# Kernel tuning notes

Measured on AMD Instinct MI355X. Metric: run time of the kernel, lower is better.

The kernel has to match this reference:

```python
import jax, jax.numpy as jnp
import numpy as np

N, C, L = 4, 256, 4096
RED, NH, CHUNK = 4, 4, 64
HB = min(L // CHUNK + (L // CHUNK) % 2, 128)  # 64 hash buckets
EPS_BN = 1e-5
EPS_NORM = 5e-5
RES_SCALE = 1.0


def _bn(x, g, b, m, v):
    # inference batchnorm over channel dim of [N, C, L]
    scale = g / jnp.sqrt(v + EPS_BN)
    return (x - m[None, :, None]) * scale[None, :, None] + b[None, :, None]


def _conv1d(x, w, pad):
    return jax.lax.conv_general_dilated(x, w, (1,), [(pad, pad)],
                                        dimension_numbers=('NCH', 'OIH', 'NCH'))


def setup_inputs() -> dict:
    key = jax.random.key(0)
    ks = jax.random.split(key, 4)
    Cr = C // RED
    return {
        'x': jax.random.normal(ks[0], (N, C, L), jnp.float32),
        'rot': jax.random.normal(ks[1], (Cr, NH, HB // 2), jnp.float32),
        'w_match': jax.random.normal(ks[2], (Cr, C, 3), jnp.float32) * 0.05,
        'bn1_g': jnp.ones((Cr,), jnp.float32), 'bn1_b': jnp.zeros((Cr,), jnp.float32),
        'bn1_m': jnp.zeros((Cr,), jnp.float32), 'bn1_v': jnp.ones((Cr,), jnp.float32),
        'w_asm': jax.random.normal(ks[3], (C, C, 1), jnp.float32) * 0.05,
        'bn2_g': jnp.ones((C,), jnp.float32), 'bn2_b': jnp.zeros((C,), jnp.float32),
        'bn2_m': jnp.zeros((C,), jnp.float32), 'bn2_v': jnp.ones((C,), jnp.float32),
        'bn3_g': jnp.ones((C,), jnp.float32), 'bn3_b': jnp.zeros((C,), jnp.float32),
        'bn3_m': jnp.zeros((C,), jnp.float32), 'bn3_v': jnp.ones((C,), jnp.float32),
    }


def reference(x, rot, w_match, bn1_g, bn1_b, bn1_m, bn1_v,
              w_asm, bn2_g, bn2_b, bn2_m, bn2_v,
              bn3_g, bn3_b, bn3_m, bn3_v):
    Cr = C // RED
    # conv_match / conv_assembly branches (conv -> BN -> ReLU)
    x_embed = jax.nn.relu(_bn(_conv1d(x, w_match, 1), bn1_g, bn1_b, bn1_m, bn1_v))  # [N,Cr,L]
    y_embed = jax.nn.relu(_bn(_conv1d(x, w_asm, 0), bn2_g, bn2_b, bn2_m, bn2_v))    # [N,C,L]
    x_embed = jnp.transpose(x_embed, (0, 2, 1))  # [N,L,Cr]
    y_embed = jnp.transpose(y_embed, (0, 2, 1))  # [N,L,C]

    # --- LSH hashing: random rotations, cat with negation, argmax bucket ---
    rv = jnp.einsum('ntf,fhi->nhti', x_embed, rot)           # [N,NH,L,HB/2]
    rv = jnp.concatenate([rv, -rv], axis=-1)                  # [N,NH,L,HB]
    codes = jnp.argmax(rv, axis=-1)                           # [N,NH,L]
    codes = codes + jnp.arange(NH, dtype=codes.dtype)[None, :, None]
    codes = codes.reshape(N, NH * L)

    indices = jnp.argsort(codes, axis=-1)
    undo_sort = jnp.argsort(indices, axis=-1)
    mod_idx = indices % L

    xs = jnp.take_along_axis(x_embed, mod_idx[:, :, None], axis=1)  # [N,NH*L,Cr]
    ys = jnp.take_along_axis(y_embed, mod_idx[:, :, None], axis=1)  # [N,NH*L,C]

    nchunks = L // CHUNK  # L divisible by CHUNK -> padding == 0
    xb = xs.reshape(N, NH, nchunks, CHUNK, Cr)
    yb = ys.reshape(N, NH, nchunks, CHUNK, C)

    # F.normalize(p=2, eps=5e-5): x / max(||x||, eps)
    nrm = jnp.linalg.norm(xb, axis=-1, keepdims=True)
    xm = xb / jnp.maximum(nrm, EPS_NORM)

    def adj(t):  # concat current, previous, next bucket along in-chunk axis
        return jnp.concatenate([t, jnp.roll(t, 1, axis=2), jnp.roll(t, -1, axis=2)], axis=3)

    xm = adj(xm)      # [N,NH,K,3*CHUNK,Cr]
    yb3 = adj(yb)     # [N,NH,K,3*CHUNK,C]

    raw = jnp.einsum('bhkie,bhkje->bhkij', xb, xm)            # [N,NH,K,CHUNK,3*CHUNK]
    lse = jax.scipy.special.logsumexp(raw, axis=-1, keepdims=True)
    score = jnp.exp(raw - lse)
    att = jnp.einsum('bhkij,bhkje->bhkie', score, yb3)        # [N,NH,K,CHUNK,C]

    att = att.reshape(N, NH * L, C)
    att = jnp.take_along_axis(att, undo_sort[:, :, None], axis=1).reshape(N, NH, L, C)
    # NOTE: original code does NOT undo-sort bucket_score; replicate faithfully
    bscore = lse.reshape(N, NH, L, 1)
    probs = jax.nn.softmax(bscore, axis=1)
    out = jnp.sum(att * probs, axis=1)                        # [N,L,C]
    out = jnp.transpose(out, (0, 2, 1))                       # [N,C,L]
    out = _bn(out, bn3_g, bn3_b, bn3_m, bn3_v) * RES_SCALE + x
    return out
```

## Files before the change

kernel.cpp:

```cpp
#include <hip/hip_runtime.h>
#include <math.h>

#define NN 4
#define CCH 256
#define LLEN 4096
#define NHEAD 4
#define NHL 16384
#define NBINS 67

typedef __attribute__((ext_vector_type(8))) short bshort8;
typedef __attribute__((ext_vector_type(4))) float f32x4;

__device__ __forceinline__ float4 f4fma(float4 a, float4 b, float4 c) {
  c.x = fmaf(a.x, b.x, c.x);
  c.y = fmaf(a.y, b.y, c.y);
  c.z = fmaf(a.z, b.z, c.z);
  c.w = fmaf(a.w, b.w, c.w);
  return c;
}
__device__ __forceinline__ float4 f4fmas(float s, float4 b, float4 c) {
  c.x = fmaf(s, b.x, c.x);
  c.y = fmaf(s, b.y, c.y);
  c.z = fmaf(s, b.z, c.z);
  c.w = fmaf(s, b.w, c.w);
  return c;
}
__device__ __forceinline__ unsigned short f2bf(float f) {
  union { float f; unsigned u; } v; v.f = f;
  unsigned r = v.u + 0x7FFF + ((v.u >> 16) & 1);
  return (unsigned short)(r >> 16);
}

__global__ __launch_bounds__(256, 2) void k_conv_match(
    const float* __restrict__ x, const float* __restrict__ w,
    const float* __restrict__ g, const float* __restrict__ b,
    const float* __restrict__ m, const float* __restrict__ v,
    float* __restrict__ xe) {
  __shared__ float xs[64 * 68];
  __shared__ float wl[64 * 193];
  const int tid = threadIdx.x;
  const int n = blockIdx.x >> 6;
  const int l0 = (blockIdx.x & 63) << 6;
  const float* xn = x + (size_t)n * CCH * LLEN;
  const int co = tid & 63;
  const int dlg = tid >> 6;
  float acc[16];
#pragma unroll
  for (int q = 0; q < 16; ++q) acc[q] = 0.f;
  for (int cc = 0; cc < 4; ++cc) {
    __syncthreads();
    for (int idx = tid; idx < 64 * 66; idx += 256) {
      int ci = idx / 66, j = idx - ci * 66;
      int l = l0 + j - 1;
      xs[ci * 68 + j] = (l >= 0 && l < LLEN) ? xn[(cc * 64 + ci) * LLEN + l] : 0.f;
    }
    for (int idx = tid; idx < 12288; idx += 256) {
      int cw = idx / 192, r = idx - cw * 192;
      wl[cw * 193 + r] = w[cw * 768 + cc * 192 + r];
    }
    __syncthreads();
    const float* wbase = &wl[co * 193];
    for (int cil = 0; cil < 64; ++cil) {
      const float* xrow = &xs[cil * 68 + dlg * 16];
      float4 p0 = ((const float4*)xrow)[0];
      float4 p1 = ((const float4*)xrow)[1];
      float4 p2 = ((const float4*)xrow)[2];
      float4 p3 = ((const float4*)xrow)[3];
      float4 p4 = ((const float4*)xrow)[4];
      float xr[20] = {p0.x,p0.y,p0.z,p0.w, p1.x,p1.y,p1.z,p1.w,
                      p2.x,p2.y,p2.z,p2.w, p3.x,p3.y,p3.z,p3.w,
                      p4.x,p4.y,p4.z,p4.w};
      float w0 = wbase[cil*3], w1 = wbase[cil*3+1], w2 = wbase[cil*3+2];
#pragma unroll
      for (int q = 0; q < 16; ++q) {
        acc[q] = fmaf(w0, xr[q], acc[q]);
        acc[q] = fmaf(w1, xr[q+1], acc[q]);
        acc[q] = fmaf(w2, xr[q+2], acc[q]);
      }
    }
  }
  float scale = g[co] * rsqrtf(v[co] + 1e-5f);
  float bias = b[co] - m[co] * scale;
  float* xo = xe + ((size_t)n * LLEN + l0) * 64 + co;
#pragma unroll
  for (int q = 0; q < 16; ++q) {
    float val = acc[q] * scale + bias;
    xo[(dlg * 16 + q) * 64] = val > 0.f ? val : 0.f;
  }
}

__global__ __launch_bounds__(256, 3) void k_conv_asm(
    const float* __restrict__ x, const float* __restrict__ w,
    const float* __restrict__ g, const float* __restrict__ b,
    const float* __restrict__ m, const float* __restrict__ v,
    float* __restrict__ ye) {
  __shared__ float xt[64 * 68];
  __shared__ float wt[64 * 132];
  const int tid = threadIdx.x;
  const int n = blockIdx.x >> 6;
  const int l0 = (blockIdx.x & 63) << 6;
  const int cg = tid & 31, lt = tid >> 5;
  float4 a0[8], a1[8];
#pragma unroll
  for (int q = 0; q < 8; ++q) { a0[q] = make_float4(0,0,0,0); a1[q] = make_float4(0,0,0,0); }
  for (int cc = 0; cc < 4; ++cc) {
    __syncthreads();
    for (int idx = tid; idx < 4096; idx += 256) {
      int ci = idx >> 6, dl = idx & 63;
      xt[ci * 68 + dl] = x[((size_t)n * 256 + cc * 64 + ci) * 4096 + l0 + dl];
    }
    for (int idx = tid; idx < 8192; idx += 256) {
      int ci = idx & 63, cl = idx >> 6;
      int c = ((cl >> 2) << 3) + (cl & 3);
      wt[ci * 132 + cl] = w[c * 256 + cc * 64 + ci];
    }
    __syncthreads();
    for (int ci = 0; ci < 64; ++ci) {
      const float4 xv0 = *(const float4*)&xt[ci * 68 + lt * 8];
      const float4 xv1 = *(const float4*)&xt[ci * 68 + lt * 8 + 4];
      const float4 w0 = *(const float4*)&wt[ci * 132 + cg * 4];
      float xl[8] = {xv0.x, xv0.y, xv0.z, xv0.w, xv1.x, xv1.y, xv1.z, xv1.w};
#pragma unroll
      for (int q = 0; q < 8; ++q) a0[q] = f4fmas(xl[q], w0, a0[q]);
    }
    __syncthreads();
    for (int idx = tid; idx < 8192; idx += 256) {
      int ci = idx & 63, cl = idx >> 6;
      int c = ((cl >> 2) << 3) + 4 + (cl & 3);
      wt[ci * 132 + cl] = w[c * 256 + cc * 64 + ci];
    }
    __syncthreads();
    for (int ci = 0; ci < 64; ++ci) {
      const float4 xv0 = *(const float4*)&xt[ci * 68 + lt * 8];
      const float4 xv1 = *(const float4*)&xt[ci * 68 + lt * 8 + 4];
      const float4 w1 = *(const float4*)&wt[ci * 132 + cg * 4];
      float xl[8] = {xv0.x, xv0.y, xv0.z, xv0.w, xv1.x, xv1.y, xv1.z, xv1.w};
#pragma unroll
      for (int q = 0; q < 8; ++q) a1[q] = f4fmas(xl[q], w1, a1[q]);
    }
  }
  const int c0 = cg * 8;
  float sc[8], bs[8];
#pragma unroll
  for (int u = 0; u < 8; ++u) {
    float s = g[c0+u] * rsqrtf(v[c0+u] + 1e-5f);
    sc[u] = s; bs[u] = b[c0+u] - m[c0+u] * s;
  }
#pragma unroll
  for (int q = 0; q < 8; ++q) {
    int l = l0 + lt * 8 + q;
    float4 o0, o1;
    o0.x = fmaxf(a0[q].x*sc[0]+bs[0], 0.f);
    o0.y = fmaxf(a0[q].y*sc[1]+bs[1], 0.f);
    o0.z = fmaxf(a0[q].z*sc[2]+bs[2], 0.f);
    o0.w = fmaxf(a0[q].w*sc[3]+bs[3], 0.f);
    o1.x = fmaxf(a1[q].x*sc[4]+bs[4], 0.f);
    o1.y = fmaxf(a1[q].y*sc[5]+bs[5], 0.f);
    o1.z = fmaxf(a1[q].z*sc[6]+bs[6], 0.f);
    o1.w = fmaxf(a1[q].w*sc[7]+bs[7], 0.f);
    float4* dst = (float4*)(ye + ((size_t)n * LLEN + l) * 256 + c0);
    dst[0] = o0; dst[1] = o1;
  }
}

__global__ __launch_bounds__(256) void k_codes(
    const float* __restrict__ xe, const float* __restrict__ rot,
    int* __restrict__ codes) {
  __shared__ float xsh[64 * 65];
  const int tid = threadIdx.x;
  const int n = blockIdx.x >> 6;
  const int t0 = (blockIdx.x & 63) << 6;
  for (int idx = tid; idx < 4096; idx += 256) {
    int tt = idx >> 6, f = idx & 63;
    xsh[tt * 65 + f] = xe[((size_t)n * LLEN + t0 + tt) * 64 + f];
  }
  __syncthreads();
  const int tt = tid & 63, h = tid >> 6;
  float rvv[32];
#pragma unroll
  for (int i = 0; i < 32; ++i) rvv[i] = 0.f;
  const float* xr = &xsh[tt * 65];
  for (int f = 0; f < 64; ++f) {
    float xf = xr[f];
    const float* rr = rot + ((f << 2) + h) * 32;
#pragma unroll
    for (int i = 0; i < 32; ++i) rvv[i] = fmaf(xf, rr[i], rvv[i]);
  }
  float best = rvv[0]; int bi = 0;
#pragma unroll
  for (int i = 1; i < 32; ++i) { if (rvv[i] > best) { best = rvv[i]; bi = i; } }
#pragma unroll
  for (int i = 0; i < 32; ++i) { float nv = -rvv[i]; if (nv > best) { best = nv; bi = 32 + i; } }
  codes[n * NHL + h * LLEN + t0 + tt] = bi + h;
}

__global__ __launch_bounds__(256) void k_hist(const int* __restrict__ codes,
                                              int* __restrict__ offs) {
  __shared__ int hist[NBINS];
  const int tid = threadIdx.x;
  const int n = blockIdx.x;
  if (tid < NBINS) hist[tid] = 0;
  __syncthreads();
  const int* cp = codes + n * NHL;
  for (int idx = tid; idx < NHL; idx += 256) atomicAdd(&hist[cp[idx]], 1);
  __syncthreads();
  if (tid == 0) {
    int s = 0;
    for (int c = 0; c < NBINS; ++c) { offs[n * (NBINS + 1) + c] = s; s += hist[c]; }
    offs[n * (NBINS + 1) + NBINS] = s;
  }
}

__global__ __launch_bounds__(64) void k_scatter(const int* __restrict__ codes,
                                                const int* __restrict__ offs,
                                                int* __restrict__ sidx,
                                                int* __restrict__ undo) {
  const int n = blockIdx.x / NBINS;
  const int c = blockIdx.x - n * NBINS;
  const int lane = threadIdx.x;
  const int* cp = codes + n * NHL;
  int base = offs[n * (NBINS + 1) + c];
  for (int ch = 0; ch < NHL / 64; ++ch) {
    int j = (ch << 6) + lane;
    int cv = cp[j];
    unsigned long long mk = __ballot(cv == c);
    if (cv == c) {
      int pos = base + __popcll(mk & ((1ull << lane) - 1ull));
      sidx[n * NHL + pos] = j;
      undo[n * NHL + j] = pos;
    }
    base += __popcll(mk);
  }
}

__global__ __launch_bounds__(256, 2) void k_att2(const float* __restrict__ xe,
                                                 const float* __restrict__ ye,
                                                 const int* __restrict__ sidx,
                                                 float* __restrict__ lseg,
                                                 float* __restrict__ att) {
  __shared__ float score[64 * 193];
  __shared__ float stg[4608];
  __shared__ int   tmap[192];
  __shared__ float rinv_c[64];
  __shared__ float psum[256];
  __shared__ float pm[256], ps[256];
  __shared__ float lse_row[64];
  const int tid = threadIdx.x;
  const int blk = blockIdx.x;
  const int n = blk >> 8, h = (blk >> 6) & 3, k = blk & 63;
  if (tid < 192) {
    int jl = tid & 63;
    int chn = (tid < 64) ? k : ((tid < 128) ? ((k + 63) & 63) : ((k + 1) & 63));
    tmap[tid] = sidx[n * NHL + h * LLEN + chn * 64 + jl] & (LLEN - 1);
  }
  __syncthreads();
  const float* xen = xe + (size_t)n * LLEN * 64;
  const int il = tid & 63, jg = tid >> 6;
  float4 xi[16];
  float ml = -1e30f, sl = 0.f;
  for (int jc = 0; jc < 3; ++jc) {
    if (jc) __syncthreads();
    {
      int r = tid >> 2, c0 = (tid & 3) * 16;
      const float4* src = (const float4*)(xen + (size_t)tmap[jc * 64 + r] * 64 + c0);
      float4* dst = (float4*)&stg[r * 68 + c0];
      dst[0] = src[0]; dst[1] = src[1]; dst[2] = src[2]; dst[3] = src[3];
    }
    __syncthreads();
    {
      int prt = tid >> 6;
      const float4* row = (const float4*)&stg[il * 68 + prt * 16];
      float s = 0.f;
#pragma unroll
      for (int u = 0; u < 4; ++u) {
        float4 vv = row[u];
        s += vv.x*vv.x + vv.y*vv.y + vv.z*vv.z + vv.w*vv.w;
      }
      psum[il * 4 + prt] = s;
    }
    __syncthreads();
    if (tid < 64) {
      float s = psum[tid*4] + psum[tid*4+1] + psum[tid*4+2] + psum[tid*4+3];
      rinv_c[tid] = 1.f / fmaxf(sqrtf(s), 5e-5f);
    }
    if (jc == 0) {
      const float4* xr = (const float4*)&stg[il * 68];
#pragma unroll
      for (int u = 0; u < 16; ++u) xi[u] = xr[u];
    }
    __syncthreads();
    for (int jj = 0; jj < 16; ++jj) {
      int jl2 = jg * 16 + jj;
      const float4* xj = (const float4*)&stg[jl2 * 68];
      float4 d4 = make_float4(0, 0, 0, 0);
#pragma unroll
      for (int u = 0; u < 16; ++u) d4 = f4fma(xi[u], xj[u], d4);
      float d = (d4.x + d4.y + d4.z + d4.w) * rinv_c[jl2];
      score[il * 193 + jc * 64 + jl2] = d;
      if (d > ml) { sl = sl * __expf(ml - d) + 1.f; ml = d; }
      else sl += __expf(d - ml);
    }
  }
  pm[il * 4 + jg] = ml; ps[il * 4 + jg] = sl;
  __syncthreads();
  if (tid < 64) {
    float m0 = pm[tid*4], m1 = pm[tid*4+1], m2 = pm[tid*4+2], m3 = pm[tid*4+3];
    float mm = fmaxf(fmaxf(m0, m1), fmaxf(m2, m3));
    float ss = ps[tid*4]  * __expf(m0 - mm) + ps[tid*4+1] * __expf(m1 - mm)
             + ps[tid*4+2] * __expf(m2 - mm) + ps[tid*4+3] * __expf(m3 - mm);
    float lv = mm + __logf(ss);
    lse_row[tid] = lv;
    lseg[n * NHL + h * LLEN + k * 64 + tid] = lv;
  }
  __syncthreads();
  float pbuf[48];
  {
    float lv = lse_row[il];
#pragma unroll
    for (int jc2 = 0; jc2 < 3; ++jc2)
#pragma unroll
      for (int jj = 0; jj < 16; ++jj)
        pbuf[jc2 * 16 + jj] = __expf(score[il * 193 + jc2 * 64 + jg * 16 + jj] - lv);
  }
  __syncthreads();
  {
    unsigned short* sb = (unsigned short*)score;
#pragma unroll
    for (int jc2 = 0; jc2 < 3; ++jc2)
#pragma unroll
      for (int jj = 0; jj < 16; ++jj) {
        int j = jc2 * 64 + jg * 16 + jj;
        sb[il * 200 + j] = f2bf(pbuf[jc2 * 16 + jj]);
      }
  }
  const int wv = tid >> 6, l = tid & 63;
  f32x4 acc[16];
#pragma unroll
  for (int ct = 0; ct < 16; ++ct) acc[ct] = (f32x4){0.f, 0.f, 0.f, 0.f};
  const unsigned short* sb = (const unsigned short*)score;
  unsigned short* ysh = (unsigned short*)stg;
  const float* yen = ye + (size_t)n * LLEN * 256;
  for (int kk = 0; kk < 6; ++kk) {
    __syncthreads();
    {
      int jl = tid & 31, c0 = (tid >> 5) * 32;
      const float4* src = (const float4*)(yen + (size_t)tmap[kk * 32 + jl] * 256 + c0);
#pragma unroll
      for (int u = 0; u < 8; ++u) {
        float4 yv = src[u];
        ysh[(c0 + u*4 + 0) * 32 + jl] = f2bf(yv.x);
        ysh[(c0 + u*4 + 1) * 32 + jl] = f2bf(yv.y);
        ysh[(c0 + u*4 + 2) * 32 + jl] = f2bf(yv.z);
        ysh[(c0 + u*4 + 3) * 32 + jl] = f2bf(yv.w);
      }
    }
    __syncthreads();
    bshort8 af = *(const bshort8*)&sb[(wv * 16 + (l & 15)) * 200 + kk * 32 + (l >> 4) * 8];
#pragma unroll
    for (int ct = 0; ct < 16; ++ct) {
      bshort8 bf = *(const bshort8*)&ysh[(ct * 16 + (l & 15)) * 32 + (l >> 4) * 8];
      acc[ct] = __builtin_amdgcn_mfma_f32_16x16x32_bf16(af, bf, acc[ct], 0, 0, 0);
    }
  }
  float* abase = att + ((size_t)n * NHL + h * LLEN + k * 64) * 256;
#pragma unroll
  for (int ct = 0; ct < 16; ++ct) {
    int c = ct * 16 + (l & 15);
    int i0 = wv * 16 + (l >> 4) * 4;
#pragma unroll
    for (int r = 0; r < 4; ++r)
      abase[(size_t)(i0 + r) * 256 + c] = acc[ct][r];
  }
}

__global__ __launch_bounds__(256, 2) void k_final3(const float* __restrict__ att,
                                                   const int* __restrict__ undo,
                                                   const float* __restrict__ lse,
                                                   const float* __restrict__ x,
                                                   const float* __restrict__ g,
                                                   const float* __restrict__ b,
                                                   const float* __restrict__ m,
                                                   const float* __restrict__ v,
                                                   float* __restrict__ out) {
  __shared__ float t[32 * 257];
  __shared__ float wts[32 * 4];
  __shared__ int   pos[32 * 4];
  const int tid = threadIdx.x;
  const int n = blockIdx.x >> 7;
  const int l0 = (blockIdx.x & 127) << 5;
  if (tid < 32) {
    int l = l0 + tid;
    float e0 = lse[n * NHL + l];
    float e1 = lse[n * NHL + LLEN + l];
    float e2 = lse[n * NHL + 2 * LLEN + l];
    float e3 = lse[n * NHL + 3 * LLEN + l];
    float mx = fmaxf(fmaxf(e0, e1), fmaxf(e2, e3));
    float x0 = __expf(e0 - mx), x1 = __expf(e1 - mx), x2 = __expf(e2 - mx), x3 = __expf(e3 - mx);
    float inv = 1.f / (x0 + x1 + x2 + x3);
    wts[tid * 4 + 0] = x0 * inv; wts[tid * 4 + 1] = x1 * inv;
    wts[tid * 4 + 2] = x2 * inv; wts[tid * 4 + 3] = x3 * inv;
    pos[tid * 4 + 0] = undo[n * NHL + l];
    pos[tid * 4 + 1] = undo[n * NHL + LLEN + l];
    pos[tid * 4 + 2] = undo[n * NHL + 2 * LLEN + l];
    pos[tid * 4 + 3] = undo[n * NHL + 3 * LLEN + l];
  }
  __syncthreads();
  {
    const int ll = tid & 31, part = tid >> 5;
    float4 acc[8];
#pragma unroll
    for (int u = 0; u < 8; ++u) acc[u] = make_float4(0, 0, 0, 0);
    const float* an = att + (size_t)n * NHL * 256;
    for (int hh = 0; hh < 4; ++hh) {
      float wvv = wts[ll * 4 + hh];
      const float4* row = (const float4*)(an + (size_t)pos[ll * 4 + hh] * 256 + part * 32);
#pragma unroll
      for (int u = 0; u < 8; ++u) acc[u] = f4fmas(wvv, row[u], acc[u]);
    }
    float4* dst = (float4*)&t[ll * 257 + part * 32];
#pragma unroll
    for (int u = 0; u < 8; ++u) dst[u] = acc[u];
  }
  __syncthreads();
  for (int idx = tid; idx < 8192; idx += 256) {
    int c = idx >> 5, dl = idx & 31;
    float s = g[c] * rsqrtf(v[c] + 1e-5f);
    float bias = b[c] - m[c] * s;
    size_t o = ((size_t)n * 256 + c) * LLEN + l0 + dl;
    out[o] = t[dl * 257 + c] * s + bias + x[o];
  }
}

extern "C" void kernel_launch(void* const* d_in, const int* in_sizes, int n_in,
                              void* d_out, int out_size, void* d_ws, size_t ws_size,
                              hipStream_t stream) {
  const float* x       = (const float*)d_in[0];
  const float* rot     = (const float*)d_in[1];
  const float* w_match = (const float*)d_in[2];
  const float* bn1_g   = (const float*)d_in[3];
  const float* bn1_b   = (const float*)d_in[4];
  const float* bn1_m   = (const float*)d_in[5];
  const float* bn1_v   = (const float*)d_in[6];
  const float* w_asm   = (const float*)d_in[7];
  const float* bn2_g   = (const float*)d_in[8];
  const float* bn2_b   = (const float*)d_in[9];
  const float* bn2_m   = (const float*)d_in[10];
  const float* bn2_v   = (const float*)d_in[11];
  const float* bn3_g   = (const float*)d_in[12];
  const float* bn3_b   = (const float*)d_in[13];
  const float* bn3_m   = (const float*)d_in[14];
  const float* bn3_v   = (const float*)d_in[15];
  float* out = (float*)d_out;

  float* ws   = (float*)d_ws;
  float* xe   = ws;
  float* ye   = xe + 1048576;
  float* att  = ye + 4194304;
  float* lse  = att + 16777216;
  int* codes  = (int*)(lse + 65536);
  int* sidx   = codes + 65536;
  int* undo   = sidx + 65536;
  int* offs   = undo + 65536;

  k_conv_match<<<256, 256, 0, stream>>>(x, w_match, bn1_g, bn1_b, bn1_m, bn1_v, xe);
  k_conv_asm<<<256, 256, 0, stream>>>(x, w_asm, bn2_g, bn2_b, bn2_m, bn2_v, ye);
  k_codes<<<256, 256, 0, stream>>>(xe, rot, codes);
  k_hist<<<NN, 256, 0, stream>>>(codes, offs);
  k_scatter<<<NN * NBINS, 64, 0, stream>>>(codes, offs, sidx, undo);
  k_att2<<<1024, 256, 0, stream>>>(xe, ye, sidx, lse, att);
  k_final3<<<NN * 128, 256, 0, stream>>>(att, undo, lse, x, bn3_g, bn3_b, bn3_m, bn3_v, out);
}
```

Measured before the change: 421.4 us.

## Shrink conv tiles for more blocks; keep attention scores in registers as bf16

Both convolution kernels now use 16-position tiles instead of 64 and launch 1024 blocks instead of 256, so more blocks fit on the GPU and the 256-block launch no longer underfills it. The cost is more redundant weight loading per output. The attention kernel keeps raw scores in registers instead of a float shared-memory buffer and writes packed bf16 probabilities directly. This cuts shared memory and drops one barrier, allowing 3 blocks per CU.

```diff
diff --git a/kernel.cpp b/kernel.cpp
--- a/kernel.cpp
+++ b/kernel.cpp
@@ -31,51 +31,48 @@
   return (unsigned short)(r >> 16);
 }
 
-__global__ __launch_bounds__(256, 2) void k_conv_match(
+__global__ __launch_bounds__(256, 4) void k_conv_match(
     const float* __restrict__ x, const float* __restrict__ w,
     const float* __restrict__ g, const float* __restrict__ b,
     const float* __restrict__ m, const float* __restrict__ v,
     float* __restrict__ xe) {
-  __shared__ float xs[64 * 68];
-  __shared__ float wl[64 * 193];
-  const int tid = threadIdx.x;
-  const int n = blockIdx.x >> 6;
-  const int l0 = (blockIdx.x & 63) << 6;
+  __shared__ float xs[64 * 20];
+  __shared__ float wl[64 * 97];
+  const int tid = threadIdx.x;
+  const int n = blockIdx.x >> 8;
+  const int l0 = (blockIdx.x & 255) << 4;
   const float* xn = x + (size_t)n * CCH * LLEN;
   const int co = tid & 63;
   const int dlg = tid >> 6;
-  float acc[16];
-#pragma unroll
-  for (int q = 0; q < 16; ++q) acc[q] = 0.f;
+  float acc[4] = {0.f, 0.f, 0.f, 0.f};
   for (int cc = 0; cc < 4; ++cc) {
-    __syncthreads();
-    for (int idx = tid; idx < 64 * 66; idx += 256) {
-      int ci = idx / 66, j = idx - ci * 66;
-      int l = l0 + j - 1;
-      xs[ci * 68 + j] = (l >= 0 && l < LLEN) ? xn[(cc * 64 + ci) * LLEN + l] : 0.f;
-    }
-    for (int idx = tid; idx < 12288; idx += 256) {
-      int cw = idx / 192, r = idx - cw * 192;
-      wl[cw * 193 + r] = w[cw * 768 + cc * 192 + r];
-    }
-    __syncthreads();
-    const float* wbase = &wl[co * 193];
-    for (int cil = 0; cil < 64; ++cil) {
-      const float* xrow = &xs[cil * 68 + dlg * 16];
-      float4 p0 = ((const float4*)xrow)[0];
-      float4 p1 = ((const float4*)xrow)[1];
-      float4 p2 = ((const float4*)xrow)[2];
-      float4 p3 = ((const float4*)xrow)[3];
-      float4 p4 = ((const float4*)xrow)[4];
-      float xr[20] = {p0.x,p0.y,p0.z,p0.w, p1.x,p1.y,p1.z,p1.w,
-                      p2.x,p2.y,p2.z,p2.w, p3.x,p3.y,p3.z,p3.w,
-                      p4.x,p4.y,p4.z,p4.w};
-      float w0 = wbase[cil*3], w1 = wbase[cil*3+1], w2 = wbase[cil*3+2];
-#pragma unroll
-      for (int q = 0; q < 16; ++q) {
-        acc[q] = fmaf(w0, xr[q], acc[q]);
-        acc[q] = fmaf(w1, xr[q+1], acc[q]);
-        acc[q] = fmaf(w2, xr[q+2], acc[q]);
+    for (int ch = 0; ch < 2; ++ch) {
+      __syncthreads();
+      if (ch == 0) {
+        for (int idx = tid; idx < 1152; idx += 256) {
+          int ci = idx / 18, j = idx - ci * 18;
+          int l = l0 + j - 1;
+          xs[ci * 20 + j] = (l >= 0 && l < LLEN) ? xn[(cc * 64 + ci) * LLEN + l] : 0.f;
+        }
+      }
+      for (int idx = tid; idx < 6144; idx += 256) {
+        int cw = idx / 96, r = idx - cw * 96;
+        wl[cw * 97 + r] = w[cw * 768 + cc * 192 + ch * 96 + r];
+      }
+      __syncthreads();
+      const float* wbase = &wl[co * 97];
+      for (int cil = 0; cil < 32; ++cil) {
+        const float* xrow = &xs[(ch * 32 + cil) * 20 + dlg * 4];
+        float4 p0 = ((const float4*)xrow)[0];
+        float4 p1 = ((const float4*)xrow)[1];
+        float xr[8] = {p0.x, p0.y, p0.z, p0.w, p1.x, p1.y, p1.z, p1.w};
+        float w0 = wbase[cil*3], w1 = wbase[cil*3+1], w2 = wbase[cil*3+2];
+#pragma unroll
+        for (int q = 0; q < 4; ++q) {
+          acc[q] = fmaf(w0, xr[q], acc[q]);
+          acc[q] = fmaf(w1, xr[q+1], acc[q]);
+          acc[q] = fmaf(w2, xr[q+2], acc[q]);
+        }
       }
     }
   }
@@ -83,31 +80,31 @@
   float bias = b[co] - m[co] * scale;
   float* xo = xe + ((size_t)n * LLEN + l0) * 64 + co;
 #pragma unroll
-  for (int q = 0; q < 16; ++q) {
+  for (int q = 0; q < 4; ++q) {
     float val = acc[q] * scale + bias;
-    xo[(dlg * 16 + q) * 64] = val > 0.f ? val : 0.f;
-  }
-}
-
-__global__ __launch_bounds__(256, 3) void k_conv_asm(
+    xo[(dlg * 4 + q) * 64] = val > 0.f ? val : 0.f;
+  }
+}
+
+__global__ __launch_bounds__(256, 4) void k_conv_asm(
     const float* __restrict__ x, const float* __restrict__ w,
     const float* __restrict__ g, const float* __restrict__ b,
     const float* __restrict__ m, const float* __restrict__ v,
     float* __restrict__ ye) {
-  __shared__ float xt[64 * 68];
+  __shared__ float xt[64 * 20];
   __shared__ float wt[64 * 132];
   const int tid = threadIdx.x;
-  const int n = blockIdx.x >> 6;
-  const int l0 = (blockIdx.x & 63) << 6;
+  const int n = blockIdx.x >> 8;
+  const int l0 = (blockIdx.x & 255) << 4;
   const int cg = tid & 31, lt = tid >> 5;
-  float4 a0[8], a1[8];
-#pragma unroll
-  for (int q = 0; q < 8; ++q) { a0[q] = make_float4(0,0,0,0); a1[q] = make_float4(0,0,0,0); }
+  float4 a0[2], a1[2];
+#pragma unroll
+  for (int q = 0; q < 2; ++q) { a0[q] = make_float4(0,0,0,0); a1[q] = make_float4(0,0,0,0); }
   for (int cc = 0; cc < 4; ++cc) {
     __syncthreads();
-    for (int idx = tid; idx < 4096; idx += 256) {
-      int ci = idx >> 6, dl = idx & 63;
-      xt[ci * 68 + dl] = x[((size_t)n * 256 + cc * 64 + ci) * 4096 + l0 + dl];
+    for (int idx = tid; idx < 1024; idx += 256) {
+      int ci = idx >> 4, dl = idx & 15;
+      xt[ci * 20 + dl] = x[((size_t)n * 256 + cc * 64 + ci) * 4096 + l0 + dl];
     }
     for (int idx = tid; idx < 8192; idx += 256) {
       int ci = idx & 63, cl = idx >> 6;
@@ -116,12 +113,10 @@
     }
     __syncthreads();
     for (int ci = 0; ci < 64; ++ci) {
-      const float4 xv0 = *(const float4*)&xt[ci * 68 + lt * 8];
-      const float4 xv1 = *(const float4*)&xt[ci * 68 + lt * 8 + 4];
+      const float2 xv = *(const float2*)&xt[ci * 20 + lt * 2];
       const float4 w0 = *(const float4*)&wt[ci * 132 + cg * 4];
-      float xl[8] = {xv0.x, xv0.y, xv0.z, xv0.w, xv1.x, xv1.y, xv1.z, xv1.w};
-#pragma unroll
-      for (int q = 0; q < 8; ++q) a0[q] = f4fmas(xl[q], w0, a0[q]);
+      a0[0] = f4fmas(xv.x, w0, a0[0]);
+      a0[1] = f4fmas(xv.y, w0, a0[1]);
     }
     __syncthreads();
     for (int idx = tid; idx < 8192; idx += 256) {
@@ -131,12 +126,10 @@
     }
     __syncthreads();
     for (int ci = 0; ci < 64; ++ci) {
-      const float4 xv0 = *(const float4*)&xt[ci * 68 + lt * 8];
-      const float4 xv1 = *(const float4*)&xt[ci * 68 + lt * 8 + 4];
+      const float2 xv = *(const float2*)&xt[ci * 20 + lt * 2];
       const float4 w1 = *(const float4*)&wt[ci * 132 + cg * 4];
-      float xl[8] = {xv0.x, xv0.y, xv0.z, xv0.w, xv1.x, xv1.y, xv1.z, xv1.w};
-#pragma unroll
-      for (int q = 0; q < 8; ++q) a1[q] = f4fmas(xl[q], w1, a1[q]);
+      a1[0] = f4fmas(xv.x, w1, a1[0]);
+      a1[1] = f4fmas(xv.y, w1, a1[1]);
     }
   }
   const int c0 = cg * 8;
@@ -147,8 +140,8 @@
     sc[u] = s; bs[u] = b[c0+u] - m[c0+u] * s;
   }
 #pragma unroll
-  for (int q = 0; q < 8; ++q) {
-    int l = l0 + lt * 8 + q;
+  for (int q = 0; q < 2; ++q) {
+    int l = l0 + lt * 2 + q;
     float4 o0, o1;
     o0.x = fmaxf(a0[q].x*sc[0]+bs[0], 0.f);
     o0.y = fmaxf(a0[q].y*sc[1]+bs[1], 0.f);
@@ -233,13 +226,13 @@
   }
 }
 
-__global__ __launch_bounds__(256, 2) void k_att2(const float* __restrict__ xe,
+__global__ __launch_bounds__(256, 3) void k_att2(const float* __restrict__ xe,
                                                  const float* __restrict__ ye,
                                                  const int* __restrict__ sidx,
                                                  float* __restrict__ lseg,
                                                  float* __restrict__ att) {
-  __shared__ float score[64 * 193];
-  __shared__ float stg[4608];
+  __shared__ unsigned short Psh[64 * 200];
+  __shared__ float stg[4352];
   __shared__ int   tmap[192];
   __shared__ float rinv_c[64];
   __shared__ float psum[256];
@@ -257,6 +250,7 @@
   const float* xen = xe + (size_t)n * LLEN * 64;
   const int il = tid & 63, jg = tid >> 6;
   float4 xi[16];
+  float pbuf[48];
   float ml = -1e30f, sl = 0.f;
   for (int jc = 0; jc < 3; ++jc) {
     if (jc) __syncthreads();
@@ -296,7 +290,7 @@
 #pragma unroll
       for (int u = 0; u < 16; ++u) d4 = f4fma(xi[u], xj[u], d4);
       float d = (d4.x + d4.y + d4.z + d4.w) * rinv_c[jl2];
-      score[il * 193 + jc * 64 + jl2] = d;
+      pbuf[jc * 16 + jj] = d;
       if (d > ml) { sl = sl * __expf(ml - d) + 1.f; ml = d; }
       else sl += __expf(d - ml);
     }
@@ -313,31 +307,22 @@
     lseg[n * NHL + h * LLEN + k * 64 + tid] = lv;
   }
   __syncthreads();
-  float pbuf[48];
   {
     float lv = lse_row[il];
+    unsigned* pw32 = (unsigned*)Psh;
 #pragma unroll
     for (int jc2 = 0; jc2 < 3; ++jc2)
 #pragma unroll
-      for (int jj = 0; jj < 16; ++jj)
-        pbuf[jc2 * 16 + jj] = __expf(score[il * 193 + jc2 * 64 + jg * 16 + jj] - lv);
-  }
-  __syncthreads();
-  {
-    unsigned short* sb = (unsigned short*)score;
-#pragma unroll
-    for (int jc2 = 0; jc2 < 3; ++jc2)
-#pragma unroll
-      for (int jj = 0; jj < 16; ++jj) {
-        int j = jc2 * 64 + jg * 16 + jj;
-        sb[il * 200 + j] = f2bf(pbuf[jc2 * 16 + jj]);
+      for (int jj = 0; jj < 16; jj += 2) {
+        unsigned lo = f2bf(__expf(pbuf[jc2 * 16 + jj]     - lv));
+        unsigned hi = f2bf(__expf(pbuf[jc2 * 16 + jj + 1] - lv));
+        pw32[(il * 200 + jc2 * 64 + jg * 16 + jj) >> 1] = lo | (hi << 16);
       }
   }
   const int wv = tid >> 6, l = tid & 63;
   f32x4 acc[16];
 #pragma unroll
   for (int ct = 0; ct < 16; ++ct) acc[ct] = (f32x4){0.f, 0.f, 0.f, 0.f};
-  const unsigned short* sb = (const unsigned short*)score;
   unsigned short* ysh = (unsigned short*)stg;
   const float* yen = ye + (size_t)n * LLEN * 256;
   for (int kk = 0; kk < 6; ++kk) {
@@ -355,7 +340,7 @@
       }
     }
     __syncthreads();
-    bshort8 af = *(const bshort8*)&sb[(wv * 16 + (l & 15)) * 200 + kk * 32 + (l >> 4) * 8];
+    bshort8 af = *(const bshort8*)&Psh[(wv * 16 + (l & 15)) * 200 + kk * 32 + (l >> 4) * 8];
 #pragma unroll
     for (int ct = 0; ct < 16; ++ct) {
       bshort8 bf = *(const bshort8*)&ysh[(ct * 16 + (l & 15)) * 32 + (l >> 4) * 8];
@@ -462,8 +447,8 @@
   int* undo   = sidx + 65536;
   int* offs   = undo + 65536;
 
-  k_conv_match<<<256, 256, 0, stream>>>(x, w_match, bn1_g, bn1_b, bn1_m, bn1_v, xe);
-  k_conv_asm<<<256, 256, 0, stream>>>(x, w_asm, bn2_g, bn2_b, bn2_m, bn2_v, ye);
+  k_conv_match<<<1024, 256, 0, stream>>>(x, w_match, bn1_g, bn1_b, bn1_m, bn1_v, xe);
+  k_conv_asm<<<1024, 256, 0, stream>>>(x, w_asm, bn2_g, bn2_b, bn2_m, bn2_v, ye);
   k_codes<<<256, 256, 0, stream>>>(xe, rot, codes);
   k_hist<<<NN, 256, 0, stream>>>(codes, offs);
   k_scatter<<<NN * NBINS, 64, 0, stream>>>(codes, offs, sidx, undo);
```

Measured after the change: 1.372 ms. 3.26x slower.
